# Kernel optimization log

Measured on AMD Instinct MI355X. Metric: run time of the kernel, lower is better.

The kernel has to match this reference:

```python
import jax, jax.numpy as jnp
import numpy as np

RMS_EPS = 1e-6


def setup_inputs() -> dict:
    key = jax.random.key(0)
    ks = jax.random.split(key, 6)
    B, S, D, F, E = 4, 2048, 1024, 4096, 8
    scale = 0.02
    return {
        "hidden_states": jax.random.normal(ks[0], (B, S, D), dtype=jnp.float32),
        "norm_weight": jnp.ones((D,), dtype=jnp.float32),
        "gate_w": jax.random.normal(ks[1], (E, D), dtype=jnp.float32) * scale,
        "w1": jax.random.normal(ks[2], (E, D, F), dtype=jnp.float32) * scale,
        "w3": jax.random.normal(ks[3], (E, D, F), dtype=jnp.float32) * scale,
        "w2": jax.random.normal(ks[4], (E, F, D), dtype=jnp.float32) * scale,
        "top_k": 2,
    }


def reference(hidden_states, norm_weight, gate_w, w1, w3, w2, top_k):
    B, S, D = hidden_states.shape
    E = gate_w.shape[0]
    # norm_fn: RMSNorm (pre-MoE norm in Mixtral block)
    x = hidden_states * jax.lax.rsqrt(jnp.mean(jnp.square(hidden_states), axis=-1, keepdims=True) + RMS_EPS)
    x = (x * norm_weight).reshape(-1, D)  # [T, D], T = B*S
    # router
    router_logits = jnp.einsum('td,ed->te', x, gate_w)  # [T, E]
    routing = jax.nn.softmax(router_logits.astype(jnp.float32), axis=-1)
    top_w, top_idx = jax.lax.top_k(routing, top_k)  # [T, k]
    top_w = top_w / jnp.sum(top_w, axis=-1, keepdims=True)
    top_w = top_w.astype(x.dtype)
    # dense-masked expert combine: tokens not routed to expert e get weight 0,
    # mathematically identical to the gather/scatter loop in the original.
    out = jnp.zeros_like(x)
    for e in range(E):  # fixed small loop over experts
        w_e = jnp.sum(jnp.where(top_idx == e, top_w, 0.0), axis=-1)  # [T]
        h = jax.nn.silu(x @ w1[e]) * (x @ w3[e])  # [T, F] SwiGLU expert
        out = out + w_e[:, None] * (h @ w2[e])
    return out.reshape(B, S, D), router_logits
```

## Files before the change

kernel.cpp:

```cpp
#include <hip/hip_runtime.h>
#include <hip/hip_bf16.h>

#define T_TOK 8192
#define D_DIM 1024
#define F_DIM 4096
#define E_NUM 8

typedef short s16x8 __attribute__((ext_vector_type(8)));
typedef float f32x4 __attribute__((ext_vector_type(4)));
typedef unsigned short u16x8 __attribute__((ext_vector_type(8)));

__device__ __forceinline__ unsigned short f2bf(float f) {
  union { float f; unsigned int u; } v; v.f = f;
  unsigned int u = v.u;
  return (unsigned short)((u + 0x7FFFu + ((u >> 16) & 1u)) >> 16);
}

__device__ __forceinline__ void async16(const void* g, void* l) {
  __builtin_amdgcn_global_load_lds((const __attribute__((address_space(1))) void*)g,
                                   (__attribute__((address_space(3))) void*)l, 16, 0, 0);
}

__global__ __launch_bounds__(256) void norm_router_kernel(
    const float* __restrict__ hs, const float* __restrict__ nw,
    const float* __restrict__ gw, unsigned short* __restrict__ xb,
    float* __restrict__ logits_out, int* __restrict__ cnt,
    int* __restrict__ ilist, float* __restrict__ wlist) {
  int t = blockIdx.x;
  int tid = threadIdx.x;
  int lane = tid & 63, wid = tid >> 6;
  float4 v = ((const float4*)(hs + (size_t)t * D_DIM))[tid];
  float ss = v.x * v.x + v.y * v.y + v.z * v.z + v.w * v.w;
#pragma unroll
  for (int o = 32; o > 0; o >>= 1) ss += __shfl_xor(ss, o);
  __shared__ float red[4];
  __shared__ float pl[4][8];
  if (lane == 0) red[wid] = ss;
  __syncthreads();
  float ms = (red[0] + red[1] + red[2] + red[3]) * (1.0f / 1024.0f);
  float rs = rsqrtf(ms + 1e-6f);
  float4 wv = ((const float4*)nw)[tid];
  float x0 = v.x * rs * wv.x, x1 = v.y * rs * wv.y;
  float x2 = v.z * rs * wv.z, x3 = v.w * rs * wv.w;
  ((ushort4*)(xb + (size_t)t * D_DIM))[tid] =
      make_ushort4(f2bf(x0), f2bf(x1), f2bf(x2), f2bf(x3));
  float p[8];
#pragma unroll
  for (int e = 0; e < 8; ++e) {
    float4 g = ((const float4*)(gw + (size_t)e * D_DIM))[tid];
    p[e] = x0 * g.x + x1 * g.y + x2 * g.z + x3 * g.w;
  }
#pragma unroll
  for (int e = 0; e < 8; ++e) {
#pragma unroll
    for (int o = 32; o > 0; o >>= 1) p[e] += __shfl_xor(p[e], o);
  }
  if (lane == 0) {
#pragma unroll
    for (int e = 0; e < 8; ++e) pl[wid][e] = p[e];
  }
  __syncthreads();
  if (tid == 0) {
    float l[8];
#pragma unroll
    for (int e = 0; e < 8; ++e) {
      l[e] = pl[0][e] + pl[1][e] + pl[2][e] + pl[3][e];
      logits_out[(size_t)t * 8 + e] = l[e];
    }
    int i0 = 0; float b0 = l[0];
#pragma unroll
    for (int e = 1; e < 8; ++e) if (l[e] > b0) { b0 = l[e]; i0 = e; }
    int i1 = (i0 == 0) ? 1 : 0; float b1 = l[i1];
#pragma unroll
    for (int e = 0; e < 8; ++e) if (e != i0 && l[e] > b1) { b1 = l[e]; i1 = e; }
    float wa = 1.0f / (1.0f + __expf(b1 - b0));
    float wb = 1.0f / (1.0f + __expf(b0 - b1));
    int p0 = atomicAdd(&cnt[i0], 1);
    ilist[i0 * T_TOK + p0] = t * 2;     wlist[i0 * T_TOK + p0] = wa;
    int p1 = atomicAdd(&cnt[i1], 1);
    ilist[i1 * T_TOK + p1] = t * 2 + 1; wlist[i1 * T_TOK + p1] = wb;
  }
}

__global__ __launch_bounds__(256) void transpose_cvt_kernel(
    const float* __restrict__ w1, const float* __restrict__ w3,
    const float* __restrict__ w2, unsigned short* __restrict__ w13t,
    unsigned short* __restrict__ w2t) {
  __shared__ unsigned short tileS[64][72];
  int bx = blockIdx.x;
  int tensor = bx >> 13;
  int e = (bx >> 10) & 7;
  int tl = bx & 1023;
  const float* src; int C, tr, tc;
  if (tensor == 0) {
    src = w1 + (size_t)e * D_DIM * F_DIM; C = F_DIM; tr = tl >> 6; tc = tl & 63;
  } else if (tensor == 1) {
    src = w3 + (size_t)e * D_DIM * F_DIM; C = F_DIM; tr = tl >> 6; tc = tl & 63;
  } else {
    src = w2 + (size_t)e * F_DIM * D_DIM; C = D_DIM; tr = tl >> 4; tc = tl & 15;
  }
  int r0 = tr * 64, c0 = tc * 64;
  int tid = threadIdx.x;
  int rr = tid >> 4, ccb = (tid & 15) * 4;
#pragma unroll
  for (int i = 0; i < 4; ++i) {
    int r = rr + i * 16;
    float4 v = *(const float4*)(src + (size_t)(r0 + r) * C + c0 + ccb);
    tileS[ccb + 0][r] = f2bf(v.x);
    tileS[ccb + 1][r] = f2bf(v.y);
    tileS[ccb + 2][r] = f2bf(v.z);
    tileS[ccb + 3][r] = f2bf(v.w);
  }
  __syncthreads();
  int row = tid >> 2, col = (tid & 3) * 16;
  unsigned short* dp;
  if (tensor < 2) {
    int f = c0 + row;
    int prow = ((f >> 6) * 128) + (f & 63) + (tensor == 1 ? 64 : 0);
    dp = w13t + ((size_t)e * 8192 + prow) * D_DIM + r0 + col;
  } else {
    dp = w2t + ((size_t)e * D_DIM + c0 + row) * F_DIM + r0 + col;
  }
  u16x8 v0, v1;
#pragma unroll
  for (int j = 0; j < 8; ++j) { v0[j] = tileS[row][col + j]; v1[j] = tileS[row][col + 8 + j]; }
  *(u16x8*)dp = v0;
  *(u16x8*)(dp + 8) = v1;
}

__global__ __launch_bounds__(256, 3) void gemm1_kernel(
    const unsigned short* __restrict__ xb, const unsigned short* __restrict__ w13t,
    unsigned short* __restrict__ H, const int* __restrict__ cnt,
    const int* __restrict__ ilist) {
  int flat = blockIdx.x;
  int W = (flat & 7) * 4096 + (flat >> 3);
  int rt = W & 63;
  int p = W >> 6;
  int ft = p & 63;
  int e = p >> 6;
  int ne = cnt[e];
  int r0 = rt * 128;
  if (r0 >= ne) return;
  __shared__ __align__(16) unsigned short As[2][128 * 32];
  __shared__ __align__(16) unsigned short Bs[2][128 * 32];
  __shared__ int toks[128];
  int tid = threadIdx.x, lane = tid & 63, w = tid >> 6;
  if (tid < 128) toks[tid] = ilist[e * T_TOK + min(r0 + tid, ne - 1)];
  __syncthreads();
  const unsigned short* bpanel = w13t + ((size_t)(e * 64 + ft) * 128) * D_DIM;
  int sr0 = w * 32 + (lane >> 2);
  int sr1 = sr0 + 16;
  int ch0 = (((lane & 3) ^ ((sr0 >> 1) & 3)) * 8);
  int ch1 = (((lane & 3) ^ ((sr1 >> 1) & 3)) * 8);
  const unsigned short* asrc0 = xb + (size_t)(toks[sr0] >> 1) * D_DIM + ch0;
  const unsigned short* asrc1 = xb + (size_t)(toks[sr1] >> 1) * D_DIM + ch1;
  const unsigned short* bsrc0 = bpanel + (size_t)sr0 * D_DIM + ch0;
  const unsigned short* bsrc1 = bpanel + (size_t)sr1 * D_DIM + ch1;
  int d0 = (w * 2 + 0) * 512 + lane * 8;
  int d1 = (w * 2 + 1) * 512 + lane * 8;
  f32x4 acc[2][8] = {};
  async16(asrc0, &As[0][d0]); async16(bsrc0, &Bs[0][d0]);
  async16(asrc1, &As[0][d1]); async16(bsrc1, &Bs[0][d1]);
  __syncthreads();
  int cur = 0;
  for (int k0 = 0; k0 < D_DIM; k0 += 32) {
    int nk = k0 + 32;
    if (nk < D_DIM) {
      async16(asrc0 + nk, &As[cur ^ 1][d0]); async16(bsrc0 + nk, &Bs[cur ^ 1][d0]);
      async16(asrc1 + nk, &As[cur ^ 1][d1]); async16(bsrc1 + nk, &Bs[cur ^ 1][d1]);
    }
    int lc = lane >> 4;
    s16x8 a[2], b[8];
#pragma unroll
    for (int m = 0; m < 2; ++m) {
      int row = w * 32 + m * 16 + (lane & 15);
      a[m] = *(const s16x8*)(&As[cur][row * 32 + ((lc ^ ((row >> 1) & 3)) * 8)]);
    }
#pragma unroll
    for (int n = 0; n < 8; ++n) {
      int row = n * 16 + (lane & 15);
      b[n] = *(const s16x8*)(&Bs[cur][row * 32 + ((lc ^ ((row >> 1) & 3)) * 8)]);
    }
#pragma unroll
    for (int m = 0; m < 2; ++m)
#pragma unroll
      for (int n = 0; n < 8; ++n)
        acc[m][n] = __builtin_amdgcn_mfma_f32_16x16x32_bf16(a[m], b[n], acc[m][n], 0, 0, 0);
    __syncthreads();
    cur ^= 1;
  }
  int g4 = lane >> 4, cl = lane & 15;
#pragma unroll
  for (int m = 0; m < 2; ++m) {
#pragma unroll
    for (int j = 0; j < 4; ++j) {
      int rloc = w * 32 + m * 16 + g4 * 4 + j;
      if (r0 + rloc < ne) {
        unsigned short* hp = H + (size_t)toks[rloc] * F_DIM + ft * 64 + cl;
#pragma unroll
        for (int n = 0; n < 4; ++n) {
          float c1 = acc[m][n][j], c3 = acc[m][n + 4][j];
          float h = c1 / (1.0f + __expf(-c1)) * c3;
          __builtin_nontemporal_store(f2bf(h), hp + n * 16);
        }
      }
    }
  }
}

__global__ __launch_bounds__(256, 3) void gemm2_kernel(
    const unsigned short* __restrict__ H, const unsigned short* __restrict__ w2t,
    const int* __restrict__ cnt, const int* __restrict__ ilist,
    const float* __restrict__ wlist, float* __restrict__ out) {
  int flat = blockIdx.x;
  int W = (flat & 7) * 512 + (flat >> 3);
  int rt = W & 63;
  int p = W >> 6;
  int n0i = p & 7;
  int e = p >> 3;
  int ne = cnt[e];
  int r0 = rt * 128;
  if (r0 >= ne) return;
  int n0 = n0i * 128;
  __shared__ __align__(16) unsigned short As[2][128 * 32];
  __shared__ __align__(16) unsigned short Bs[2][128 * 32];
  __shared__ int toks[128];
  __shared__ float wts[128];
  int tid = threadIdx.x, lane = tid & 63, w = tid >> 6;
  if (tid < 128) {
    int idx = e * T_TOK + min(r0 + tid, ne - 1);
    toks[tid] = ilist[idx];
    wts[tid] = wlist[idx];
  }
  __syncthreads();
  const unsigned short* bpanel = w2t + ((size_t)e * D_DIM + n0) * F_DIM;
  int sr0 = w * 32 + (lane >> 2);
  int sr1 = sr0 + 16;
  int ch0 = (((lane & 3) ^ ((sr0 >> 1) & 3)) * 8);
  int ch1 = (((lane & 3) ^ ((sr1 >> 1) & 3)) * 8);
  const unsigned short* asrc0 = H + (size_t)toks[sr0] * F_DIM + ch0;
  const unsigned short* asrc1 = H + (size_t)toks[sr1] * F_DIM + ch1;
  const unsigned short* bsrc0 = bpanel + (size_t)sr0 * F_DIM + ch0;
  const unsigned short* bsrc1 = bpanel + (size_t)sr1 * F_DIM + ch1;
  int d0 = (w * 2 + 0) * 512 + lane * 8;
  int d1 = (w * 2 + 1) * 512 + lane * 8;
  f32x4 acc[4][4] = {};
  int wr = w >> 1, wc = w & 1;
  async16(asrc0, &As[0][d0]); async16(bsrc0, &Bs[0][d0]);
  async16(asrc1, &As[0][d1]); async16(bsrc1, &Bs[0][d1]);
  __syncthreads();
  int cur = 0;
  for (int k0 = 0; k0 < F_DIM; k0 += 32) {
    int nk = k0 + 32;
    if (nk < F_DIM) {
      async16(asrc0 + nk, &As[cur ^ 1][d0]); async16(bsrc0 + nk, &Bs[cur ^ 1][d0]);
      async16(asrc1 + nk, &As[cur ^ 1][d1]); async16(bsrc1 + nk, &Bs[cur ^ 1][d1]);
    }
    int lc = lane >> 4;
    s16x8 a[4], b[4];
#pragma unroll
    for (int m = 0; m < 4; ++m) {
      int row = wr * 64 + m * 16 + (lane & 15);
      a[m] = *(const s16x8*)(&As[cur][row * 32 + ((lc ^ ((row >> 1) & 3)) * 8)]);
    }
#pragma unroll
    for (int n = 0; n < 4; ++n) {
      int row = wc * 64 + n * 16 + (lane & 15);
      b[n] = *(const s16x8*)(&Bs[cur][row * 32 + ((lc ^ ((row >> 1) & 3)) * 8)]);
    }
#pragma unroll
    for (int m = 0; m < 4; ++m)
#pragma unroll
      for (int n = 0; n < 4; ++n)
        acc[m][n] = __builtin_amdgcn_mfma_f32_16x16x32_bf16(a[m], b[n], acc[m][n], 0, 0, 0);
    __syncthreads();
    cur ^= 1;
  }
  int g4 = lane >> 4, cl = lane & 15;
#pragma unroll
  for (int m = 0; m < 4; ++m) {
#pragma unroll
    for (int j = 0; j < 4; ++j) {
      int rloc = wr * 64 + m * 16 + g4 * 4 + j;
      if (r0 + rloc < ne) {
        int tok = toks[rloc] >> 1;
        float ww = wts[rloc];
        float* op = out + (size_t)tok * D_DIM + n0 + wc * 64 + cl;
#pragma unroll
        for (int n = 0; n < 4; ++n)
          unsafeAtomicAdd(op + n * 16, ww * acc[m][n][j]);
      }
    }
  }
}

extern "C" void kernel_launch(void* const* d_in, const int* in_sizes, int n_in,
                              void* d_out, int out_size, void* d_ws, size_t ws_size,
                              hipStream_t stream) {
  const float* hs = (const float*)d_in[0];
  const float* nw = (const float*)d_in[1];
  const float* gw = (const float*)d_in[2];
  const float* w1 = (const float*)d_in[3];
  const float* w3 = (const float*)d_in[4];
  const float* w2 = (const float*)d_in[5];
  float* out = (float*)d_out;
  float* logits_out = out + (size_t)T_TOK * D_DIM;

  char* ws = (char*)d_ws;
  unsigned short* xb   = (unsigned short*)(ws);
  unsigned short* w13t = (unsigned short*)(ws + 16777216ull);
  unsigned short* w2t  = (unsigned short*)(ws + 150994944ull);
  unsigned short* H    = (unsigned short*)(ws + 218103808ull);
  int*   ilist = (int*)(ws + 352321536ull);
  float* wlist = (float*)(ws + 352583680ull);
  int*   cnt   = (int*)(ws + 352845824ull);

  hipMemsetAsync(d_out, 0, (size_t)out_size * sizeof(float), stream);
  hipMemsetAsync(cnt, 0, E_NUM * sizeof(int), stream);
  norm_router_kernel<<<T_TOK, 256, 0, stream>>>(hs, nw, gw, xb, logits_out, cnt, ilist, wlist);
  transpose_cvt_kernel<<<3 * E_NUM * 1024, 256, 0, stream>>>(w1, w3, w2, w13t, w2t);
  gemm1_kernel<<<E_NUM * 64 * 64, 256, 0, stream>>>(xb, w13t, H, cnt, ilist);
  gemm2_kernel<<<E_NUM * 64 * 8, 256, 0, stream>>>(H, w2t, cnt, ilist, wlist, out);
}
```

Baseline: 966.7 us.

## Triple-buffer LDS tiles with one barrier per k-step in expert GEMMs

Both expert GEMM kernels move from double to triple LDS buffering, keeping two tiles of async global-to-LDS loads in flight. A manual vmcnt wait plus a single s_barrier per iteration replaces the trailing __syncthreads. This is meant to hide global load latency and cut synchronisation overhead, at the cost of more LDS per block, which may reduce occupancy. The SwiGLU output store in gemm1 also drops the nontemporal hint and becomes a plain store.

```diff
diff --git a/kernel.cpp b/kernel.cpp
--- a/kernel.cpp
+++ b/kernel.cpp
@@ -141,8 +141,8 @@
   int ne = cnt[e];
   int r0 = rt * 128;
   if (r0 >= ne) return;
-  __shared__ __align__(16) unsigned short As[2][128 * 32];
-  __shared__ __align__(16) unsigned short Bs[2][128 * 32];
+  __shared__ __align__(16) unsigned short As[3 * 4096];
+  __shared__ __align__(16) unsigned short Bs[3 * 4096];
   __shared__ int toks[128];
   int tid = threadIdx.x, lane = tid & 63, w = tid >> 6;
   if (tid < 128) toks[tid] = ilist[e * T_TOK + min(r0 + tid, ne - 1)];
@@ -159,35 +159,41 @@
   int d0 = (w * 2 + 0) * 512 + lane * 8;
   int d1 = (w * 2 + 1) * 512 + lane * 8;
   f32x4 acc[2][8] = {};
-  async16(asrc0, &As[0][d0]); async16(bsrc0, &Bs[0][d0]);
-  async16(asrc1, &As[0][d1]); async16(bsrc1, &Bs[0][d1]);
-  __syncthreads();
-  int cur = 0;
-  for (int k0 = 0; k0 < D_DIM; k0 += 32) {
-    int nk = k0 + 32;
-    if (nk < D_DIM) {
-      async16(asrc0 + nk, &As[cur ^ 1][d0]); async16(bsrc0 + nk, &Bs[cur ^ 1][d0]);
-      async16(asrc1 + nk, &As[cur ^ 1][d1]); async16(bsrc1 + nk, &Bs[cur ^ 1][d1]);
-    }
+  async16(asrc0, &As[d0]); async16(bsrc0, &Bs[d0]);
+  async16(asrc1, &As[d1]); async16(bsrc1, &Bs[d1]);
+  async16(asrc0 + 32, &As[4096 + d0]); async16(bsrc0 + 32, &Bs[4096 + d0]);
+  async16(asrc1 + 32, &As[4096 + d1]); async16(bsrc1 + 32, &Bs[4096 + d1]);
+  int bt = 0;
+  for (int t = 0; t < 32; ++t) {
+    if (t < 31) asm volatile("s_waitcnt vmcnt(4)" ::: "memory");
+    else        asm volatile("s_waitcnt vmcnt(0)" ::: "memory");
+    __builtin_amdgcn_s_barrier();
+    if (t + 2 < 32) {
+      int nb = bt + 2; if (nb >= 3) nb -= 3;
+      int nk = (t + 2) * 32;
+      async16(asrc0 + nk, &As[nb * 4096 + d0]); async16(bsrc0 + nk, &Bs[nb * 4096 + d0]);
+      async16(asrc1 + nk, &As[nb * 4096 + d1]); async16(bsrc1 + nk, &Bs[nb * 4096 + d1]);
+    }
+    const unsigned short* Ab = &As[bt * 4096];
+    const unsigned short* Bb = &Bs[bt * 4096];
     int lc = lane >> 4;
     s16x8 a[2], b[8];
 #pragma unroll
     for (int m = 0; m < 2; ++m) {
       int row = w * 32 + m * 16 + (lane & 15);
-      a[m] = *(const s16x8*)(&As[cur][row * 32 + ((lc ^ ((row >> 1) & 3)) * 8)]);
+      a[m] = *(const s16x8*)(&Ab[row * 32 + ((lc ^ ((row >> 1) & 3)) * 8)]);
     }
 #pragma unroll
     for (int n = 0; n < 8; ++n) {
       int row = n * 16 + (lane & 15);
-      b[n] = *(const s16x8*)(&Bs[cur][row * 32 + ((lc ^ ((row >> 1) & 3)) * 8)]);
+      b[n] = *(const s16x8*)(&Bb[row * 32 + ((lc ^ ((row >> 1) & 3)) * 8)]);
     }
 #pragma unroll
     for (int m = 0; m < 2; ++m)
 #pragma unroll
       for (int n = 0; n < 8; ++n)
         acc[m][n] = __builtin_amdgcn_mfma_f32_16x16x32_bf16(a[m], b[n], acc[m][n], 0, 0, 0);
-    __syncthreads();
-    cur ^= 1;
+    if (++bt == 3) bt = 0;
   }
   int g4 = lane >> 4, cl = lane & 15;
 #pragma unroll
@@ -201,7 +207,7 @@
         for (int n = 0; n < 4; ++n) {
           float c1 = acc[m][n][j], c3 = acc[m][n + 4][j];
           float h = c1 / (1.0f + __expf(-c1)) * c3;
-          __builtin_nontemporal_store(f2bf(h), hp + n * 16);
+          hp[n * 16] = f2bf(h);
         }
       }
     }
@@ -222,8 +228,8 @@
   int r0 = rt * 128;
   if (r0 >= ne) return;
   int n0 = n0i * 128;
-  __shared__ __align__(16) unsigned short As[2][128 * 32];
-  __shared__ __align__(16) unsigned short Bs[2][128 * 32];
+  __shared__ __align__(16) unsigned short As[3 * 4096];
+  __shared__ __align__(16) unsigned short Bs[3 * 4096];
   __shared__ int toks[128];
   __shared__ float wts[128];
   int tid = threadIdx.x, lane = tid & 63, w = tid >> 6;
@@ -246,35 +252,41 @@
   int d1 = (w * 2 + 1) * 512 + lane * 8;
   f32x4 acc[4][4] = {};
   int wr = w >> 1, wc = w & 1;
-  async16(asrc0, &As[0][d0]); async16(bsrc0, &Bs[0][d0]);
-  async16(asrc1, &As[0][d1]); async16(bsrc1, &Bs[0][d1]);
-  __syncthreads();
-  int cur = 0;
-  for (int k0 = 0; k0 < F_DIM; k0 += 32) {
-    int nk = k0 + 32;
-    if (nk < F_DIM) {
-      async16(asrc0 + nk, &As[cur ^ 1][d0]); async16(bsrc0 + nk, &Bs[cur ^ 1][d0]);
-      async16(asrc1 + nk, &As[cur ^ 1][d1]); async16(bsrc1 + nk, &Bs[cur ^ 1][d1]);
-    }
+  async16(asrc0, &As[d0]); async16(bsrc0, &Bs[d0]);
+  async16(asrc1, &As[d1]); async16(bsrc1, &Bs[d1]);
+  async16(asrc0 + 32, &As[4096 + d0]); async16(bsrc0 + 32, &Bs[4096 + d0]);
+  async16(asrc1 + 32, &As[4096 + d1]); async16(bsrc1 + 32, &Bs[4096 + d1]);
+  int bt = 0;
+  for (int t = 0; t < 128; ++t) {
+    if (t < 127) asm volatile("s_waitcnt vmcnt(4)" ::: "memory");
+    else         asm volatile("s_waitcnt vmcnt(0)" ::: "memory");
+    __builtin_amdgcn_s_barrier();
+    if (t + 2 < 128) {
+      int nb = bt + 2; if (nb >= 3) nb -= 3;
+      int nk = (t + 2) * 32;
+      async16(asrc0 + nk, &As[nb * 4096 + d0]); async16(bsrc0 + nk, &Bs[nb * 4096 + d0]);
+      async16(asrc1 + nk, &As[nb * 4096 + d1]); async16(bsrc1 + nk, &Bs[nb * 4096 + d1]);
+    }
+    const unsigned short* Ab = &As[bt * 4096];
+    const unsigned short* Bb = &Bs[bt * 4096];
     int lc = lane >> 4;
     s16x8 a[4], b[4];
 #pragma unroll
     for (int m = 0; m < 4; ++m) {
       int row = wr * 64 + m * 16 + (lane & 15);
-      a[m] = *(const s16x8*)(&As[cur][row * 32 + ((lc ^ ((row >> 1) & 3)) * 8)]);
+      a[m] = *(const s16x8*)(&Ab[row * 32 + ((lc ^ ((row >> 1) & 3)) * 8)]);
     }
 #pragma unroll
     for (int n = 0; n < 4; ++n) {
       int row = wc * 64 + n * 16 + (lane & 15);
-      b[n] = *(const s16x8*)(&Bs[cur][row * 32 + ((lc ^ ((row >> 1) & 3)) * 8)]);
+      b[n] = *(const s16x8*)(&Bb[row * 32 + ((lc ^ ((row >> 1) & 3)) * 8)]);
     }
 #pragma unroll
     for (int m = 0; m < 4; ++m)
 #pragma unroll
       for (int n = 0; n < 4; ++n)
         acc[m][n] = __builtin_amdgcn_mfma_f32_16x16x32_bf16(a[m], b[n], acc[m][n], 0, 0, 0);
-    __syncthreads();
-    cur ^= 1;
+    if (++bt == 3) bt = 0;
   }
   int g4 = lane >> 4, cl = lane & 15;
 #pragma unroll
```

Result: faster. 939.1 us (-2.9%).

## Enlarge GEMM tiles to 128x256 with triple-buffered LDS pipeline and expert-interleaved grid

Applied to the files above, without the earlier changes.

Both expert GEMMs move from 128x128 tiles to 128x256 tiles, with 4x8 MFMA fragments per wave. The LDS pipeline goes from double to triple buffering, synchronised with explicit vmcnt waits and raw barriers so two stages of loads stay in flight. The block-to-work mapping now interleaves experts, and occupancy drops to 2 blocks per CU. Larger tiles mean more operand reuse and fewer global loads per FLOP, at the cost of higher register and LDS pressure and coarser tail granularity. The gemm1 output store also changes from nontemporal to a normal store.

```diff
diff --git a/kernel.cpp b/kernel.cpp
--- a/kernel.cpp
+++ b/kernel.cpp
@@ -128,102 +128,131 @@
   *(u16x8*)(dp + 8) = v1;
 }
 
-__global__ __launch_bounds__(256, 3) void gemm1_kernel(
+__global__ __launch_bounds__(256, 2) void gemm1_kernel(
     const unsigned short* __restrict__ xb, const unsigned short* __restrict__ w13t,
     unsigned short* __restrict__ H, const int* __restrict__ cnt,
     const int* __restrict__ ilist) {
   int flat = blockIdx.x;
-  int W = (flat & 7) * 4096 + (flat >> 3);
-  int rt = W & 63;
-  int p = W >> 6;
-  int ft = p & 63;
-  int e = p >> 6;
+  int e = flat & 7;
+  int work = flat >> 3;
+  int rt = work & 63;
+  int ft = work >> 6;
   int ne = cnt[e];
   int r0 = rt * 128;
   if (r0 >= ne) return;
-  __shared__ __align__(16) unsigned short As[2][128 * 32];
-  __shared__ __align__(16) unsigned short Bs[2][128 * 32];
+  __shared__ __align__(16) unsigned short As[3 * 4096];
+  __shared__ __align__(16) unsigned short Bs[3 * 8192];
   __shared__ int toks[128];
   int tid = threadIdx.x, lane = tid & 63, w = tid >> 6;
   if (tid < 128) toks[tid] = ilist[e * T_TOK + min(r0 + tid, ne - 1)];
   __syncthreads();
-  const unsigned short* bpanel = w13t + ((size_t)(e * 64 + ft) * 128) * D_DIM;
-  int sr0 = w * 32 + (lane >> 2);
-  int sr1 = sr0 + 16;
-  int ch0 = (((lane & 3) ^ ((sr0 >> 1) & 3)) * 8);
-  int ch1 = (((lane & 3) ^ ((sr1 >> 1) & 3)) * 8);
-  const unsigned short* asrc0 = xb + (size_t)(toks[sr0] >> 1) * D_DIM + ch0;
-  const unsigned short* asrc1 = xb + (size_t)(toks[sr1] >> 1) * D_DIM + ch1;
-  const unsigned short* bsrc0 = bpanel + (size_t)sr0 * D_DIM + ch0;
-  const unsigned short* bsrc1 = bpanel + (size_t)sr1 * D_DIM + ch1;
-  int d0 = (w * 2 + 0) * 512 + lane * 8;
-  int d1 = (w * 2 + 1) * 512 + lane * 8;
-  f32x4 acc[2][8] = {};
-  async16(asrc0, &As[0][d0]); async16(bsrc0, &Bs[0][d0]);
-  async16(asrc1, &As[0][d1]); async16(bsrc1, &Bs[0][d1]);
-  __syncthreads();
-  int cur = 0;
-  for (int k0 = 0; k0 < D_DIM; k0 += 32) {
-    int nk = k0 + 32;
-    if (nk < D_DIM) {
-      async16(asrc0 + nk, &As[cur ^ 1][d0]); async16(bsrc0 + nk, &Bs[cur ^ 1][d0]);
-      async16(asrc1 + nk, &As[cur ^ 1][d1]); async16(bsrc1 + nk, &Bs[cur ^ 1][d1]);
-    }
-    int lc = lane >> 4;
-    s16x8 a[2], b[8];
-#pragma unroll
-    for (int m = 0; m < 2; ++m) {
-      int row = w * 32 + m * 16 + (lane & 15);
-      a[m] = *(const s16x8*)(&As[cur][row * 32 + ((lc ^ ((row >> 1) & 3)) * 8)]);
-    }
-#pragma unroll
-    for (int n = 0; n < 8; ++n) {
-      int row = n * 16 + (lane & 15);
-      b[n] = *(const s16x8*)(&Bs[cur][row * 32 + ((lc ^ ((row >> 1) & 3)) * 8)]);
-    }
-#pragma unroll
-    for (int m = 0; m < 2; ++m)
-#pragma unroll
-      for (int n = 0; n < 8; ++n)
-        acc[m][n] = __builtin_amdgcn_mfma_f32_16x16x32_bf16(a[m], b[n], acc[m][n], 0, 0, 0);
-    __syncthreads();
-    cur ^= 1;
-  }
+  const unsigned short* bpanel = w13t + ((size_t)e * 8192 + ft * 256) * D_DIM;
+  int la = lane >> 2, lc4 = lane & 3;
+  int ra0 = w * 32 + la, ra1 = ra0 + 16;
+  const unsigned short* ap0 = xb + (size_t)(toks[ra0] >> 1) * D_DIM + ((lc4 ^ ((ra0 >> 1) & 3)) * 8);
+  const unsigned short* ap1 = xb + (size_t)(toks[ra1] >> 1) * D_DIM + ((lc4 ^ ((ra1 >> 1) & 3)) * 8);
+  int da0 = ra0 * 32 + lc4 * 8;
+  int da1 = ra1 * 32 + lc4 * 8;
+  int rb0 = w * 64 + la, rb1 = rb0 + 16, rb2 = rb0 + 32, rb3 = rb0 + 48;
+  const unsigned short* bp0 = bpanel + (size_t)rb0 * D_DIM + ((lc4 ^ ((rb0 >> 1) & 3)) * 8);
+  const unsigned short* bp1 = bpanel + (size_t)rb1 * D_DIM + ((lc4 ^ ((rb1 >> 1) & 3)) * 8);
+  const unsigned short* bp2 = bpanel + (size_t)rb2 * D_DIM + ((lc4 ^ ((rb2 >> 1) & 3)) * 8);
+  const unsigned short* bp3 = bpanel + (size_t)rb3 * D_DIM + ((lc4 ^ ((rb3 >> 1) & 3)) * 8);
+  int db0 = rb0 * 32 + lc4 * 8, db1 = rb1 * 32 + lc4 * 8;
+  int db2 = rb2 * 32 + lc4 * 8, db3 = rb3 * 32 + lc4 * 8;
+  int wr = w >> 1, wc = w & 1;
+  int lr = lane & 15, lc = lane >> 4;
+  int aoff[4], boff[8];
+#pragma unroll
+  for (int m = 0; m < 4; ++m) {
+    int row = wr * 64 + m * 16 + lr;
+    aoff[m] = row * 32 + ((lc ^ ((row >> 1) & 3)) * 8);
+  }
+#pragma unroll
+  for (int n = 0; n < 8; ++n) {
+    int row = wc * 128 + n * 16 + lr;
+    boff[n] = row * 32 + ((lc ^ ((row >> 1) & 3)) * 8);
+  }
+  f32x4 acc[4][8] = {};
+  async16(ap0, &As[da0]); async16(ap1, &As[da1]);
+  async16(bp0, &Bs[db0]); async16(bp1, &Bs[db1]);
+  async16(bp2, &Bs[db2]); async16(bp3, &Bs[db3]);
+  async16(ap0 + 32, &As[4096 + da0]); async16(ap1 + 32, &As[4096 + da1]);
+  async16(bp0 + 32, &Bs[8192 + db0]); async16(bp1 + 32, &Bs[8192 + db1]);
+  async16(bp2 + 32, &Bs[8192 + db2]); async16(bp3 + 32, &Bs[8192 + db3]);
+
+#define G1_STEP(T_, BUF_, VMC_, DOST_)                                          \
+  {                                                                             \
+    asm volatile("s_waitcnt vmcnt(" VMC_ ")" ::: "memory");                     \
+    __builtin_amdgcn_s_barrier();                                               \
+    if (DOST_) {                                                                \
+      int nk = ((T_) + 2) * 32;                                                 \
+      async16(ap0 + nk, &As[(((BUF_) + 2) % 3) * 4096 + da0]);                  \
+      async16(ap1 + nk, &As[(((BUF_) + 2) % 3) * 4096 + da1]);                  \
+      async16(bp0 + nk, &Bs[(((BUF_) + 2) % 3) * 8192 + db0]);                  \
+      async16(bp1 + nk, &Bs[(((BUF_) + 2) % 3) * 8192 + db1]);                  \
+      async16(bp2 + nk, &Bs[(((BUF_) + 2) % 3) * 8192 + db2]);                  \
+      async16(bp3 + nk, &Bs[(((BUF_) + 2) % 3) * 8192 + db3]);                  \
+    }                                                                           \
+    {                                                                           \
+      const unsigned short* Ab = &As[(BUF_) * 4096];                            \
+      const unsigned short* Bb = &Bs[(BUF_) * 8192];                            \
+      s16x8 a[4], b[8];                                                         \
+      _Pragma("unroll") for (int m = 0; m < 4; ++m)                             \
+          a[m] = *(const s16x8*)(Ab + aoff[m]);                                 \
+      _Pragma("unroll") for (int n = 0; n < 8; ++n)                             \
+          b[n] = *(const s16x8*)(Bb + boff[n]);                                 \
+      _Pragma("unroll") for (int m = 0; m < 4; ++m)                             \
+          _Pragma("unroll") for (int n = 0; n < 8; ++n)                         \
+              acc[m][n] = __builtin_amdgcn_mfma_f32_16x16x32_bf16(              \
+                  a[m], b[n], acc[m][n], 0, 0, 0);                              \
+    }                                                                           \
+  }
+
+  for (int tb = 0; tb < 30; tb += 3) {
+    G1_STEP(tb, 0, "6", 1)
+    G1_STEP(tb + 1, 1, "6", 1)
+    G1_STEP(tb + 2, 2, "6", 1)
+  }
+  G1_STEP(30, 0, "6", 0)
+  G1_STEP(31, 1, "0", 0)
+#undef G1_STEP
+
   int g4 = lane >> 4, cl = lane & 15;
-#pragma unroll
-  for (int m = 0; m < 2; ++m) {
+  int fbase = (2 * ft + wc) * 64;
+#pragma unroll
+  for (int m = 0; m < 4; ++m) {
 #pragma unroll
     for (int j = 0; j < 4; ++j) {
-      int rloc = w * 32 + m * 16 + g4 * 4 + j;
+      int rloc = wr * 64 + m * 16 + g4 * 4 + j;
       if (r0 + rloc < ne) {
-        unsigned short* hp = H + (size_t)toks[rloc] * F_DIM + ft * 64 + cl;
+        unsigned short* hp = H + (size_t)toks[rloc] * F_DIM + fbase + cl;
 #pragma unroll
         for (int n = 0; n < 4; ++n) {
           float c1 = acc[m][n][j], c3 = acc[m][n + 4][j];
           float h = c1 / (1.0f + __expf(-c1)) * c3;
-          __builtin_nontemporal_store(f2bf(h), hp + n * 16);
+          hp[n * 16] = f2bf(h);
         }
       }
     }
   }
 }
 
-__global__ __launch_bounds__(256, 3) void gemm2_kernel(
+__global__ __launch_bounds__(256, 2) void gemm2_kernel(
     const unsigned short* __restrict__ H, const unsigned short* __restrict__ w2t,
     const int* __restrict__ cnt, const int* __restrict__ ilist,
     const float* __restrict__ wlist, float* __restrict__ out) {
   int flat = blockIdx.x;
-  int W = (flat & 7) * 512 + (flat >> 3);
-  int rt = W & 63;
-  int p = W >> 6;
-  int n0i = p & 7;
-  int e = p >> 3;
+  int e = flat & 7;
+  int work = flat >> 3;
+  int rt = work & 63;
+  int n0i = work >> 6;
   int ne = cnt[e];
   int r0 = rt * 128;
   if (r0 >= ne) return;
-  int n0 = n0i * 128;
-  __shared__ __align__(16) unsigned short As[2][128 * 32];
-  __shared__ __align__(16) unsigned short Bs[2][128 * 32];
+  int n0 = n0i * 256;
+  __shared__ __align__(16) unsigned short As[3 * 4096];
+  __shared__ __align__(16) unsigned short Bs[3 * 8192];
   __shared__ int toks[128];
   __shared__ float wts[128];
   int tid = threadIdx.x, lane = tid & 63, w = tid >> 6;
@@ -234,48 +263,77 @@
   }
   __syncthreads();
   const unsigned short* bpanel = w2t + ((size_t)e * D_DIM + n0) * F_DIM;
-  int sr0 = w * 32 + (lane >> 2);
-  int sr1 = sr0 + 16;
-  int ch0 = (((lane & 3) ^ ((sr0 >> 1) & 3)) * 8);
-  int ch1 = (((lane & 3) ^ ((sr1 >> 1) & 3)) * 8);
-  const unsigned short* asrc0 = H + (size_t)toks[sr0] * F_DIM + ch0;
-  const unsigned short* asrc1 = H + (size_t)toks[sr1] * F_DIM + ch1;
-  const unsigned short* bsrc0 = bpanel + (size_t)sr0 * F_DIM + ch0;
-  const unsigned short* bsrc1 = bpanel + (size_t)sr1 * F_DIM + ch1;
-  int d0 = (w * 2 + 0) * 512 + lane * 8;
-  int d1 = (w * 2 + 1) * 512 + lane * 8;
-  f32x4 acc[4][4] = {};
+  int la = lane >> 2, lc4 = lane & 3;
+  int ra0 = w * 32 + la, ra1 = ra0 + 16;
+  const unsigned short* ap0 = H + (size_t)toks[ra0] * F_DIM + ((lc4 ^ ((ra0 >> 1) & 3)) * 8);
+  const unsigned short* ap1 = H + (size_t)toks[ra1] * F_DIM + ((lc4 ^ ((ra1 >> 1) & 3)) * 8);
+  int da0 = ra0 * 32 + lc4 * 8;
+  int da1 = ra1 * 32 + lc4 * 8;
+  int rb0 = w * 64 + la, rb1 = rb0 + 16, rb2 = rb0 + 32, rb3 = rb0 + 48;
+  const unsigned short* bp0 = bpanel + (size_t)rb0 * F_DIM + ((lc4 ^ ((rb0 >> 1) & 3)) * 8);
+  const unsigned short* bp1 = bpanel + (size_t)rb1 * F_DIM + ((lc4 ^ ((rb1 >> 1) & 3)) * 8);
+  const unsigned short* bp2 = bpanel + (size_t)rb2 * F_DIM + ((lc4 ^ ((rb2 >> 1) & 3)) * 8);
+  const unsigned short* bp3 = bpanel + (size_t)rb3 * F_DIM + ((lc4 ^ ((rb3 >> 1) & 3)) * 8);
+  int db0 = rb0 * 32 + lc4 * 8, db1 = rb1 * 32 + lc4 * 8;
+  int db2 = rb2 * 32 + lc4 * 8, db3 = rb3 * 32 + lc4 * 8;
   int wr = w >> 1, wc = w & 1;
-  async16(asrc0, &As[0][d0]); async16(bsrc0, &Bs[0][d0]);
-  async16(asrc1, &As[0][d1]); async16(bsrc1, &Bs[0][d1]);
-  __syncthreads();
-  int cur = 0;
-  for (int k0 = 0; k0 < F_DIM; k0 += 32) {
-    int nk = k0 + 32;
-    if (nk < F_DIM) {
-      async16(asrc0 + nk, &As[cur ^ 1][d0]); async16(bsrc0 + nk, &Bs[cur ^ 1][d0]);
-      async16(asrc1 + nk, &As[cur ^ 1][d1]); async16(bsrc1 + nk, &Bs[cur ^ 1][d1]);
-    }
-    int lc = lane >> 4;
-    s16x8 a[4], b[4];
-#pragma unroll
-    for (int m = 0; m < 4; ++m) {
-      int row = wr * 64 + m * 16 + (lane & 15);
-      a[m] = *(const s16x8*)(&As[cur][row * 32 + ((lc ^ ((row >> 1) & 3)) * 8)]);
-    }
-#pragma unroll
-    for (int n = 0; n < 4; ++n) {
-      int row = wc * 64 + n * 16 + (lane & 15);
-      b[n] = *(const s16x8*)(&Bs[cur][row * 32 + ((lc ^ ((row >> 1) & 3)) * 8)]);
-    }
-#pragma unroll
-    for (int m = 0; m < 4; ++m)
-#pragma unroll
-      for (int n = 0; n < 4; ++n)
-        acc[m][n] = __builtin_amdgcn_mfma_f32_16x16x32_bf16(a[m], b[n], acc[m][n], 0, 0, 0);
-    __syncthreads();
-    cur ^= 1;
-  }
+  int lr = lane & 15, lc = lane >> 4;
+  int aoff[4], boff[8];
+#pragma unroll
+  for (int m = 0; m < 4; ++m) {
+    int row = wr * 64 + m * 16 + lr;
+    aoff[m] = row * 32 + ((lc ^ ((row >> 1) & 3)) * 8);
+  }
+#pragma unroll
+  for (int n = 0; n < 8; ++n) {
+    int row = wc * 128 + n * 16 + lr;
+    boff[n] = row * 32 + ((lc ^ ((row >> 1) & 3)) * 8);
+  }
+  f32x4 acc[4][8] = {};
+  async16(ap0, &As[da0]); async16(ap1, &As[da1]);
+  async16(bp0, &Bs[db0]); async16(bp1, &Bs[db1]);
+  async16(bp2, &Bs[db2]); async16(bp3, &Bs[db3]);
+  async16(ap0 + 32, &As[4096 + da0]); async16(ap1 + 32, &As[4096 + da1]);
+  async16(bp0 + 32, &Bs[8192 + db0]); async16(bp1 + 32, &Bs[8192 + db1]);
+  async16(bp2 + 32, &Bs[8192 + db2]); async16(bp3 + 32, &Bs[8192 + db3]);
+
+#define G2_STEP(T_, BUF_, VMC_, DOST_)                                          \
+  {                                                                             \
+    asm volatile("s_waitcnt vmcnt(" VMC_ ")" ::: "memory");                     \
+    __builtin_amdgcn_s_barrier();                                               \
+    if (DOST_) {                                                                \
+      int nk = ((T_) + 2) * 32;                                                 \
+      async16(ap0 + nk, &As[(((BUF_) + 2) % 3) * 4096 + da0]);                  \
+      async16(ap1 + nk, &As[(((BUF_) + 2) % 3) * 4096 + da1]);                  \
+      async16(bp0 + nk, &Bs[(((BUF_) + 2) % 3) * 8192 + db0]);                  \
+      async16(bp1 + nk, &Bs[(((BUF_) + 2) % 3) * 8192 + db1]);                  \
+      async16(bp2 + nk, &Bs[(((BUF_) + 2) % 3) * 8192 + db2]);                  \
+      async16(bp3 + nk, &Bs[(((BUF_) + 2) % 3) * 8192 + db3]);                  \
+    }                                                                           \
+    {                                                                           \
+      const unsigned short* Ab = &As[(BUF_) * 4096];                            \
+      const unsigned short* Bb = &Bs[(BUF_) * 8192];                            \
+      s16x8 a[4], b[8];                                                         \
+      _Pragma("unroll") for (int m = 0; m < 4; ++m)                             \
+          a[m] = *(const s16x8*)(Ab + aoff[m]);                                 \
+      _Pragma("unroll") for (int n = 0; n < 8; ++n)                             \
+          b[n] = *(const s16x8*)(Bb + boff[n]);                                 \
+      _Pragma("unroll") for (int m = 0; m < 4; ++m)                             \
+          _Pragma("unroll") for (int n = 0; n < 8; ++n)                         \
+              acc[m][n] = __builtin_amdgcn_mfma_f32_16x16x32_bf16(              \
+                  a[m], b[n], acc[m][n], 0, 0, 0);                              \
+    }                                                                           \
+  }
+
+  for (int tb = 0; tb < 126; tb += 3) {
+    G2_STEP(tb, 0, "6", 1)
+    G2_STEP(tb + 1, 1, "6", 1)
+    G2_STEP(tb + 2, 2, "6", 1)
+  }
+  G2_STEP(126, 0, "6", 0)
+  G2_STEP(127, 1, "0", 0)
+#undef G2_STEP
+
   int g4 = lane >> 4, cl = lane & 15;
 #pragma unroll
   for (int m = 0; m < 4; ++m) {
@@ -285,9 +343,9 @@
       if (r0 + rloc < ne) {
         int tok = toks[rloc] >> 1;
         float ww = wts[rloc];
-        float* op = out + (size_t)tok * D_DIM + n0 + wc * 64 + cl;
-#pragma unroll
-        for (int n = 0; n < 4; ++n)
+        float* op = out + (size_t)tok * D_DIM + n0 + wc * 128 + cl;
+#pragma unroll
+        for (int n = 0; n < 8; ++n)
           unsafeAtomicAdd(op + n * 16, ww * acc[m][n][j]);
       }
     }
@@ -319,6 +377,6 @@
   hipMemsetAsync(cnt, 0, E_NUM * sizeof(int), stream);
   norm_router_kernel<<<T_TOK, 256, 0, stream>>>(hs, nw, gw, xb, logits_out, cnt, ilist, wlist);
   transpose_cvt_kernel<<<3 * E_NUM * 1024, 256, 0, stream>>>(w1, w3, w2, w13t, w2t);
-  gemm1_kernel<<<E_NUM * 64 * 64, 256, 0, stream>>>(xb, w13t, H, cnt, ilist);
-  gemm2_kernel<<<E_NUM * 64 * 8, 256, 0, stream>>>(H, w2t, cnt, ilist, wlist, out);
-}
+  gemm1_kernel<<<E_NUM * 64 * 32, 256, 0, stream>>>(xb, w13t, H, cnt, ilist);
+  gemm2_kernel<<<E_NUM * 64 * 4, 256, 0, stream>>>(H, w2t, cnt, ilist, wlist, out);
+}
```

New measurement: 975.8 us. No clear change (+0.9%).
